# Kernel tuning notes

Hardware: AMD Instinct MI355X
Metric: run time of the kernel (lower is better)

The kernel has to match this reference:

```python
import jax, jax.numpy as jnp
import numpy as np

NUM_HEADS = 6

def setup_inputs() -> dict:
    key = jax.random.key(0)
    ks = jax.random.split(key, 6)
    B_, N, C = 4096, 64, 192
    nW = 4096
    return {
        "x": jax.random.normal(ks[0], (B_, N, C), dtype=jnp.float32),
        "mask": jax.random.normal(ks[1], (nW, N, N), dtype=jnp.float32),
        "qkv_w": jax.random.normal(ks[2], (3 * C, C), dtype=jnp.float32) * 0.02,
        "qkv_b": jax.random.normal(ks[3], (3 * C,), dtype=jnp.float32) * 0.02,
        "proj_w": jax.random.normal(ks[4], (C, C), dtype=jnp.float32) * 0.02,
        "proj_b": jax.random.normal(ks[5], (C,), dtype=jnp.float32) * 0.02,
    }

def reference(x, mask, qkv_w, qkv_b, proj_w, proj_b):
    B_, N, C = x.shape
    H = NUM_HEADS
    hd = C // H
    scale = hd ** -0.5
    qkv = (x @ qkv_w.T + qkv_b).reshape(B_, N, 3, H, hd)
    qkv = jnp.transpose(qkv, (2, 0, 3, 1, 4))  # [3, B_, H, N, hd]
    q, k, v = qkv[0], qkv[1], qkv[2]
    attn = jnp.einsum('bhnd,bhmd->bhnm', q * scale, k)  # [B_, H, N, N]
    nW = mask.shape[0]
    # additive relative/shift mask broadcast over image batch and heads
    attn = attn.reshape(B_ // nW, nW, H, N, N) + mask[None, :, None, :, :]
    attn = attn.reshape(B_, H, N, N)
    attn = jax.nn.softmax(attn, axis=-1)
    out = jnp.einsum('bhnm,bhmd->bhnd', attn, v)  # [B_, H, N, hd]
    out = jnp.transpose(out, (0, 2, 1, 3)).reshape(B_, N, C)
    return out @ proj_w.T + proj_b
```

## Files before the change

kernel.cpp:

```cpp
#include <hip/hip_runtime.h>
#include <hip/hip_bf16.h>
#include <stdint.h>


#define NTOK 64
#define CDIM 192
#define KVROW 72

typedef __attribute__((ext_vector_type(4))) float f32x4;
typedef __attribute__((ext_vector_type(8))) short bf16x8;

__device__ __forceinline__ short f2bf(float f) {
  __hip_bfloat16 h = __float2bfloat16(f);
  return *reinterpret_cast<short*>(&h);
}
__device__ __forceinline__ uint32_t pack2(float a, float b) {
  __hip_bfloat162 h2;
  h2.x = __float2bfloat16(a);
  h2.y = __float2bfloat16(b);
  return *reinterpret_cast<uint32_t*>(&h2);
}

__device__ __forceinline__ bf16x8 xpose(uint32_t A0, uint32_t A1,
                                        uint32_t B0, uint32_t B1,
                                        int s0, int s1, int hiSel) {
  uint32_t w[4];
  uint32_t a, b;
  a = (uint32_t)__shfl((int)A0, s0); b = (uint32_t)__shfl((int)B0, s0); w[0] = hiSel ? b : a;
  a = (uint32_t)__shfl((int)A1, s0); b = (uint32_t)__shfl((int)B1, s0); w[1] = hiSel ? b : a;
  a = (uint32_t)__shfl((int)A0, s1); b = (uint32_t)__shfl((int)B0, s1); w[2] = hiSel ? b : a;
  a = (uint32_t)__shfl((int)A1, s1); b = (uint32_t)__shfl((int)B1, s1); w[3] = hiSel ? b : a;
  return *reinterpret_cast<bf16x8*>(w);
}

#define GLOAD16(g, l) __builtin_amdgcn_global_load_lds( \
    (const __attribute__((address_space(1))) void*)(g), \
    (__attribute__((address_space(3))) void*)(l), 16, 0, 0)

__global__ void wconv_kernel(const float* __restrict__ qkv_w,
                             const float* __restrict__ proj_w,
                             short* __restrict__ ws) {
  const int r = blockIdx.x, c = threadIdx.x;
  int chunk, lr;
  float val;
  if (r < 192)      { chunk = r >> 6;                     lr = r & 63;          val = qkv_w[r * CDIM + c]; }
  else if (r < 384) { int q = r - 192; chunk = 3 + 2 * (q >> 6); lr = q & 63;   val = qkv_w[r * CDIM + c]; }
  else if (r < 576) { int q = r - 384; chunk = 4 + 2 * (q >> 6); lr = q & 63;   val = qkv_w[r * CDIM + c]; }
  else              { int q = r - 576; chunk = 9 + (q >> 6);     lr = q & 63;   val = proj_w[q * CDIM + c]; }
  const int s = c >> 3, lo = c & 7;
  const int sp = (s & 24) | ((s ^ lr) & 7);
  ws[chunk * 12288 + lr * CDIM + sp * 8 + lo] = f2bf(val);
}

__device__ __forceinline__ void stage_issue(short* __restrict__ wbuf,
                                            const short* __restrict__ src, int tid) {
  const int w = tid >> 6, lane = tid & 63;
  #pragma unroll
  for (int it = 0; it < 6; ++it) {
    const int cidx = it * 4 + w;
    GLOAD16(src + cidx * 512 + lane * 8, wbuf + cidx * 512);
  }
}

__global__ __launch_bounds__(256, 4)
void winattn_kernel(const float* __restrict__ x, const float* __restrict__ mask,
                    const short* __restrict__ ws,
                    const float* __restrict__ qkv_b, const float* __restrict__ proj_b,
                    float* __restrict__ out) {
  __shared__ __align__(16) short wbuf[64 * CDIM];
  __shared__ __align__(16) short khv[NTOK * KVROW];

  const int b    = blockIdx.x;
  const int tid  = threadIdx.x;
  const int lane = tid & 63;
  const int l16  = lane & 15;
  const int g4   = lane >> 4;
  const int m0   = (tid >> 6) * 16;
  const float scale = 0.17677669529663687f;
  const int s0 = (((2 * g4) & 3) << 4) + l16;
  const int s1 = (((2 * g4 + 1) & 3) << 4) + l16;
  const int hiSel = g4 >> 1;

  int soff[6];
  #pragma unroll
  for (int ks = 0; ks < 6; ++ks) {
    const int s = ks * 4 + g4;
    soff[ks] = ((s & 24) | ((s ^ l16) & 7)) << 3;
  }

  stage_issue(wbuf, ws, tid);

  const float* xr = x + (size_t)b * (NTOK * CDIM) + (m0 + l16) * CDIM;
  bf16x8 af[6];
  #pragma unroll
  for (int ks = 0; ks < 6; ++ks) {
    const float4 v0 = *reinterpret_cast<const float4*>(xr + ks * 32 + g4 * 8);
    const float4 v1 = *reinterpret_cast<const float4*>(xr + ks * 32 + g4 * 8 + 4);
    uint32_t t[4];
    t[0] = pack2(v0.x, v0.y); t[1] = pack2(v0.z, v0.w);
    t[2] = pack2(v1.x, v1.y); t[3] = pack2(v1.z, v1.w);
    af[ks] = *reinterpret_cast<bf16x8*>(t);
  }
  const float* mrowl = mask + (size_t)b * (NTOK * NTOK) + (m0 + l16) * NTOK;

  __syncthreads();

  bf16x8 aq[6];
  #pragma unroll
  for (int c = 0; c < 3; ++c) {
    uint32_t u[4][2];
    #pragma unroll
    for (int lct = 0; lct < 4; ++lct) {
      f32x4 acc = {0.f, 0.f, 0.f, 0.f};
      #pragma unroll
      for (int ks = 0; ks < 6; ++ks) {
        bf16x8 wf = *reinterpret_cast<const bf16x8*>(wbuf + (lct * 16 + l16) * CDIM + soff[ks]);
        acc = __builtin_amdgcn_mfma_f32_16x16x32_bf16(wf, af[ks], acc, 0, 0, 0);
      }
      const float4 bq = *reinterpret_cast<const float4*>(qkv_b + 64 * c + 16 * lct + 4 * g4);
      u[lct][0] = pack2((acc[0] + bq.x) * scale, (acc[1] + bq.y) * scale);
      u[lct][1] = pack2((acc[2] + bq.z) * scale, (acc[3] + bq.w) * scale);
    }
    __syncthreads();
    stage_issue(wbuf, ws + (c < 2 ? (c + 1) : 3) * 12288, tid);
    aq[2 * c]     = xpose(u[0][0], u[0][1], u[1][0], u[1][1], s0, s1, hiSel);
    aq[2 * c + 1] = xpose(u[2][0], u[2][1], u[3][0], u[3][1], s0, s1, hiSel);
    __syncthreads();
  }

  bf16x8 of[6];
  #pragma unroll
  for (int p = 0; p < 3; ++p) {
    #pragma unroll
    for (int lct = 0; lct < 4; ++lct) {
      f32x4 acc = {0.f, 0.f, 0.f, 0.f};
      #pragma unroll
      for (int ks = 0; ks < 6; ++ks) {
        bf16x8 wf = *reinterpret_cast<const bf16x8*>(wbuf + (lct * 16 + l16) * CDIM + soff[ks]);
        acc = __builtin_amdgcn_mfma_f32_16x16x32_bf16(wf, af[ks], acc, 0, 0, 0);
      }
      const float4 bk4 = *reinterpret_cast<const float4*>(qkv_b + 192 + 64 * p + 16 * lct + 4 * g4);
      uint2 kw;
      kw.x = pack2(acc[0] + bk4.x, acc[1] + bk4.y);
      kw.y = pack2(acc[2] + bk4.z, acc[3] + bk4.w);
      *reinterpret_cast<uint2*>(khv + (m0 + l16) * KVROW + 16 * lct + 4 * g4) = kw;
    }
    __syncthreads();
    stage_issue(wbuf, ws + (4 + 2 * p) * 12288, tid);

    float4 mreg[4];
    #pragma unroll
    for (int rt = 0; rt < 4; ++rt)
      mreg[rt] = *reinterpret_cast<const float4*>(mrowl + 16 * rt + 4 * g4);

    bf16x8 bp[2][2];
    #pragma unroll
    for (int e = 0; e < 2; ++e) {
      float pr[4][4];
      float rmax = -1e30f;
      #pragma unroll
      for (int rt = 0; rt < 4; ++rt) {
        bf16x8 bk = *reinterpret_cast<const bf16x8*>(khv + (rt * 16 + l16) * KVROW + 32 * e + g4 * 8);
        f32x4 z = {0.f, 0.f, 0.f, 0.f};
        f32x4 s = __builtin_amdgcn_mfma_f32_16x16x32_bf16(bk, aq[2 * p + e], z, 0, 0, 0);
        pr[rt][0] = s[0] + mreg[rt].x; pr[rt][1] = s[1] + mreg[rt].y;
        pr[rt][2] = s[2] + mreg[rt].z; pr[rt][3] = s[3] + mreg[rt].w;
        #pragma unroll
        for (int i = 0; i < 4; ++i) rmax = fmaxf(rmax, pr[rt][i]);
      }
      rmax = fmaxf(rmax, __shfl_xor(rmax, 16));
      rmax = fmaxf(rmax, __shfl_xor(rmax, 32));
      float rsum = 0.f;
      #pragma unroll
      for (int rt = 0; rt < 4; ++rt)
        #pragma unroll
        for (int i = 0; i < 4; ++i) { pr[rt][i] = __expf(pr[rt][i] - rmax); rsum += pr[rt][i]; }
      rsum += __shfl_xor(rsum, 16);
      rsum += __shfl_xor(rsum, 32);
      const float rinv = 1.f / rsum;
      uint32_t wpk[4][2];
      #pragma unroll
      for (int rt = 0; rt < 4; ++rt) {
        wpk[rt][0] = pack2(pr[rt][0] * rinv, pr[rt][1] * rinv);
        wpk[rt][1] = pack2(pr[rt][2] * rinv, pr[rt][3] * rinv);
      }
      bp[e][0] = xpose(wpk[0][0], wpk[0][1], wpk[1][0], wpk[1][1], s0, s1, hiSel);
      bp[e][1] = xpose(wpk[2][0], wpk[2][1], wpk[3][0], wpk[3][1], s0, s1, hiSel);
    }
    __syncthreads();

    #pragma unroll
    for (int lct = 0; lct < 4; ++lct) {
      f32x4 acc = {0.f, 0.f, 0.f, 0.f};
      #pragma unroll
      for (int ks = 0; ks < 6; ++ks) {
        bf16x8 wf = *reinterpret_cast<const bf16x8*>(wbuf + (lct * 16 + l16) * CDIM + soff[ks]);
        acc = __builtin_amdgcn_mfma_f32_16x16x32_bf16(af[ks], wf, acc, 0, 0, 0);
      }
      const float bv = qkv_b[384 + 64 * p + 16 * lct + l16];
      uint2 vw;
      vw.x = pack2(acc[0] + bv, acc[1] + bv);
      vw.y = pack2(acc[2] + bv, acc[3] + bv);
      *reinterpret_cast<uint2*>(khv + (16 * lct + l16) * KVROW + m0 + 4 * g4) = vw;
    }
    __syncthreads();
    stage_issue(wbuf, ws + (p < 2 ? (5 + 2 * p) : 9) * 12288, tid);

    #pragma unroll
    for (int e = 0; e < 2; ++e) {
      uint32_t uo[2][2];
      #pragma unroll
      for (int ct2 = 0; ct2 < 2; ++ct2) {
        const short* vb = khv + (32 * e + 16 * ct2 + l16) * KVROW;
        bf16x8 bv1 = *reinterpret_cast<const bf16x8*>(vb + g4 * 8);
        bf16x8 bv2 = *reinterpret_cast<const bf16x8*>(vb + 32 + g4 * 8);
        f32x4 acc = {0.f, 0.f, 0.f, 0.f};
        acc = __builtin_amdgcn_mfma_f32_16x16x32_bf16(bv1, bp[e][0], acc, 0, 0, 0);
        acc = __builtin_amdgcn_mfma_f32_16x16x32_bf16(bv2, bp[e][1], acc, 0, 0, 0);
        uo[ct2][0] = pack2(acc[0], acc[1]);
        uo[ct2][1] = pack2(acc[2], acc[3]);
      }
      of[2 * p + e] = xpose(uo[0][0], uo[0][1], uo[1][0], uo[1][1], s0, s1, hiSel);
    }
    __syncthreads();
  }

  float* og = out + (size_t)b * (NTOK * CDIM);
  #pragma unroll
  for (int c = 0; c < 3; ++c) {
    f32x4 acc[4];
    #pragma unroll
    for (int lct = 0; lct < 4; ++lct) {
      f32x4 a = {0.f, 0.f, 0.f, 0.f};
      #pragma unroll
      for (int ks = 0; ks < 6; ++ks) {
        bf16x8 wf = *reinterpret_cast<const bf16x8*>(wbuf + (lct * 16 + l16) * CDIM + soff[ks]);
        a = __builtin_amdgcn_mfma_f32_16x16x32_bf16(of[ks], wf, a, 0, 0, 0);
      }
      acc[lct] = a;
    }
    if (c < 2) {
      __syncthreads();
      stage_issue(wbuf, ws + (10 + c) * 12288, tid);
    }
    #pragma unroll
    for (int lct = 0; lct < 4; ++lct) {
      const int cc = 64 * c + 16 * lct + l16;
      const float pb = proj_b[cc];
      #pragma unroll
      for (int i = 0; i < 4; ++i)
        og[(m0 + 4 * g4 + i) * CDIM + cc] = acc[lct][i] + pb;
    }
    if (c < 2) __syncthreads();
  }
}

extern "C" void kernel_launch(void* const* d_in, const int* in_sizes, int n_in,
                              void* d_out, int out_size, void* d_ws, size_t ws_size,
                              hipStream_t stream) {
  const float* x      = (const float*)d_in[0];
  const float* mask   = (const float*)d_in[1];
  const float* qkv_w  = (const float*)d_in[2];
  const float* qkv_b  = (const float*)d_in[3];
  const float* proj_w = (const float*)d_in[4];
  const float* proj_b = (const float*)d_in[5];
  float* out = (float*)d_out;

  short* ws = (short*)d_ws;

  wconv_kernel<<<768, 192, 0, stream>>>(qkv_w, proj_w, ws);
  winattn_kernel<<<4096, 256, 0, stream>>>(x, mask, ws, qkv_b, proj_b, out);
}
```

Measured before the change: 243.4 us.

## Double-buffer 32-row weight chunks and pipeline per-head attention with PV overlap

Splits each 64-row staged weight chunk into two 32-row halves held in ping-pong LDS buffers, so the next chunk's global-to-LDS load overlaps compute on the current one. The attention loop now runs per head instead of per head pair, with a double-buffered V-transpose area, and defers each head's PV product into the next iteration to cut barriers. LDS use is roughly the same, but there are more loop iterations, more syncthreads calls and more small load issues, which could offset the overlap gain.

```diff
diff --git a/kernel.cpp b/kernel.cpp
--- a/kernel.cpp
+++ b/kernel.cpp
@@ -5,7 +5,8 @@
 
 #define NTOK 64
 #define CDIM 192
-#define KVROW 72
+#define KROW 40
+#define VROW 72
 
 typedef __attribute__((ext_vector_type(4))) float f32x4;
 typedef __attribute__((ext_vector_type(8))) short bf16x8;
@@ -43,22 +44,22 @@
   const int r = blockIdx.x, c = threadIdx.x;
   int chunk, lr;
   float val;
-  if (r < 192)      { chunk = r >> 6;                     lr = r & 63;          val = qkv_w[r * CDIM + c]; }
-  else if (r < 384) { int q = r - 192; chunk = 3 + 2 * (q >> 6); lr = q & 63;   val = qkv_w[r * CDIM + c]; }
-  else if (r < 576) { int q = r - 384; chunk = 4 + 2 * (q >> 6); lr = q & 63;   val = qkv_w[r * CDIM + c]; }
-  else              { int q = r - 576; chunk = 9 + (q >> 6);     lr = q & 63;   val = proj_w[q * CDIM + c]; }
+  if (r < 192)      { chunk = r >> 5;                        lr = r & 31;         val = qkv_w[r * CDIM + c]; }
+  else if (r < 384) { int q = r - 192; chunk = 6 + 2 * (q >> 5); lr = q & 31;     val = qkv_w[r * CDIM + c]; }
+  else if (r < 576) { int q = r - 384; chunk = 7 + 2 * (q >> 5); lr = q & 31;     val = qkv_w[r * CDIM + c]; }
+  else              { int q = r - 576; chunk = 18 + (q >> 5);    lr = q & 31;     val = proj_w[q * CDIM + c]; }
   const int s = c >> 3, lo = c & 7;
   const int sp = (s & 24) | ((s ^ lr) & 7);
-  ws[chunk * 12288 + lr * CDIM + sp * 8 + lo] = f2bf(val);
-}
-
-__device__ __forceinline__ void stage_issue(short* __restrict__ wbuf,
-                                            const short* __restrict__ src, int tid) {
+  ws[chunk * 6144 + lr * CDIM + sp * 8 + lo] = f2bf(val);
+}
+
+__device__ __forceinline__ void stage32(short* __restrict__ dst,
+                                        const short* __restrict__ src, int tid) {
   const int w = tid >> 6, lane = tid & 63;
   #pragma unroll
-  for (int it = 0; it < 6; ++it) {
+  for (int it = 0; it < 3; ++it) {
     const int cidx = it * 4 + w;
-    GLOAD16(src + cidx * 512 + lane * 8, wbuf + cidx * 512);
+    GLOAD16(src + cidx * 512 + lane * 8, dst + cidx * 512);
   }
 }
 
@@ -67,8 +68,10 @@
                     const short* __restrict__ ws,
                     const float* __restrict__ qkv_b, const float* __restrict__ proj_b,
                     float* __restrict__ out) {
-  __shared__ __align__(16) short wbuf[64 * CDIM];
-  __shared__ __align__(16) short khv[NTOK * KVROW];
+  __shared__ __align__(16) short wbA[32 * CDIM];
+  __shared__ __align__(16) short wbB[32 * CDIM];
+  __shared__ __align__(16) short kh[NTOK * KROW];
+  __shared__ __align__(16) short vth[2][32 * VROW];
 
   const int b    = blockIdx.x;
   const int tid  = threadIdx.x;
@@ -88,7 +91,8 @@
     soff[ks] = ((s & 24) | ((s ^ l16) & 7)) << 3;
   }
 
-  stage_issue(wbuf, ws, tid);
+  stage32(wbA, ws, tid);
+  stage32(wbB, ws + 6144, tid);
 
   const float* xr = x + (size_t)b * (NTOK * CDIM) + (m0 + l16) * CDIM;
   bf16x8 af[6];
@@ -107,64 +111,88 @@
 
   bf16x8 aq[6];
   #pragma unroll
-  for (int c = 0; c < 3; ++c) {
-    uint32_t u[4][2];
-    #pragma unroll
-    for (int lct = 0; lct < 4; ++lct) {
-      f32x4 acc = {0.f, 0.f, 0.f, 0.f};
-      #pragma unroll
-      for (int ks = 0; ks < 6; ++ks) {
-        bf16x8 wf = *reinterpret_cast<const bf16x8*>(wbuf + (lct * 16 + l16) * CDIM + soff[ks]);
+  for (int c = 0; c < 6; ++c) {
+    short* wb = (c & 1) ? wbB : wbA;
+    uint32_t u[2][2];
+    #pragma unroll
+    for (int lct = 0; lct < 2; ++lct) {
+      f32x4 acc = {0.f, 0.f, 0.f, 0.f};
+      #pragma unroll
+      for (int ks = 0; ks < 6; ++ks) {
+        bf16x8 wf = *reinterpret_cast<const bf16x8*>(wb + (lct * 16 + l16) * CDIM + soff[ks]);
         acc = __builtin_amdgcn_mfma_f32_16x16x32_bf16(wf, af[ks], acc, 0, 0, 0);
       }
-      const float4 bq = *reinterpret_cast<const float4*>(qkv_b + 64 * c + 16 * lct + 4 * g4);
+      const float4 bq = *reinterpret_cast<const float4*>(qkv_b + 32 * c + 16 * lct + 4 * g4);
       u[lct][0] = pack2((acc[0] + bq.x) * scale, (acc[1] + bq.y) * scale);
       u[lct][1] = pack2((acc[2] + bq.z) * scale, (acc[3] + bq.w) * scale);
     }
+    aq[c] = xpose(u[0][0], u[0][1], u[1][0], u[1][1], s0, s1, hiSel);
     __syncthreads();
-    stage_issue(wbuf, ws + (c < 2 ? (c + 1) : 3) * 12288, tid);
-    aq[2 * c]     = xpose(u[0][0], u[0][1], u[1][0], u[1][1], s0, s1, hiSel);
-    aq[2 * c + 1] = xpose(u[2][0], u[2][1], u[3][0], u[3][1], s0, s1, hiSel);
-    __syncthreads();
+    stage32(wb, ws + (c + 2) * 6144, tid);
   }
 
   bf16x8 of[6];
-  #pragma unroll
-  for (int p = 0; p < 3; ++p) {
-    #pragma unroll
-    for (int lct = 0; lct < 4; ++lct) {
-      f32x4 acc = {0.f, 0.f, 0.f, 0.f};
-      #pragma unroll
-      for (int ks = 0; ks < 6; ++ks) {
-        bf16x8 wf = *reinterpret_cast<const bf16x8*>(wbuf + (lct * 16 + l16) * CDIM + soff[ks]);
+  bf16x8 bpa, bpb;
+  #pragma unroll
+  for (int h = 0; h < 6; ++h) {
+    #pragma unroll
+    for (int lct = 0; lct < 2; ++lct) {
+      f32x4 acc = {0.f, 0.f, 0.f, 0.f};
+      #pragma unroll
+      for (int ks = 0; ks < 6; ++ks) {
+        bf16x8 wf = *reinterpret_cast<const bf16x8*>(wbA + (lct * 16 + l16) * CDIM + soff[ks]);
         acc = __builtin_amdgcn_mfma_f32_16x16x32_bf16(wf, af[ks], acc, 0, 0, 0);
       }
-      const float4 bk4 = *reinterpret_cast<const float4*>(qkv_b + 192 + 64 * p + 16 * lct + 4 * g4);
+      const float4 bk4 = *reinterpret_cast<const float4*>(qkv_b + 192 + 32 * h + 16 * lct + 4 * g4);
       uint2 kw;
       kw.x = pack2(acc[0] + bk4.x, acc[1] + bk4.y);
       kw.y = pack2(acc[2] + bk4.z, acc[3] + bk4.w);
-      *reinterpret_cast<uint2*>(khv + (m0 + l16) * KVROW + 16 * lct + 4 * g4) = kw;
+      *reinterpret_cast<uint2*>(kh + (m0 + l16) * KROW + 16 * lct + 4 * g4) = kw;
+    }
+    if (h > 0) {
+      const int vp = (h - 1) & 1;
+      uint32_t uo[2][2];
+      #pragma unroll
+      for (int ct2 = 0; ct2 < 2; ++ct2) {
+        const short* vb = vth[vp] + (16 * ct2 + l16) * VROW;
+        bf16x8 bv1 = *reinterpret_cast<const bf16x8*>(vb + g4 * 8);
+        bf16x8 bv2 = *reinterpret_cast<const bf16x8*>(vb + 32 + g4 * 8);
+        f32x4 acc = {0.f, 0.f, 0.f, 0.f};
+        acc = __builtin_amdgcn_mfma_f32_16x16x32_bf16(bv1, bpa, acc, 0, 0, 0);
+        acc = __builtin_amdgcn_mfma_f32_16x16x32_bf16(bv2, bpb, acc, 0, 0, 0);
+        uo[ct2][0] = pack2(acc[0], acc[1]);
+        uo[ct2][1] = pack2(acc[2], acc[3]);
+      }
+      of[h - 1] = xpose(uo[0][0], uo[0][1], uo[1][0], uo[1][1], s0, s1, hiSel);
     }
     __syncthreads();
-    stage_issue(wbuf, ws + (4 + 2 * p) * 12288, tid);
-
-    float4 mreg[4];
-    #pragma unroll
-    for (int rt = 0; rt < 4; ++rt)
-      mreg[rt] = *reinterpret_cast<const float4*>(mrowl + 16 * rt + 4 * g4);
-
-    bf16x8 bp[2][2];
-    #pragma unroll
-    for (int e = 0; e < 2; ++e) {
+    stage32(wbA, ws + (8 + 2 * h) * 6144, tid);
+
+    #pragma unroll
+    for (int lct = 0; lct < 2; ++lct) {
+      f32x4 acc = {0.f, 0.f, 0.f, 0.f};
+      #pragma unroll
+      for (int ks = 0; ks < 6; ++ks) {
+        bf16x8 wf = *reinterpret_cast<const bf16x8*>(wbB + (lct * 16 + l16) * CDIM + soff[ks]);
+        acc = __builtin_amdgcn_mfma_f32_16x16x32_bf16(af[ks], wf, acc, 0, 0, 0);
+      }
+      const float bv = qkv_b[384 + 32 * h + 16 * lct + l16];
+      uint2 vw;
+      vw.x = pack2(acc[0] + bv, acc[1] + bv);
+      vw.y = pack2(acc[2] + bv, acc[3] + bv);
+      *reinterpret_cast<uint2*>(vth[h & 1] + (16 * lct + l16) * VROW + m0 + 4 * g4) = vw;
+    }
+    {
       float pr[4][4];
       float rmax = -1e30f;
       #pragma unroll
       for (int rt = 0; rt < 4; ++rt) {
-        bf16x8 bk = *reinterpret_cast<const bf16x8*>(khv + (rt * 16 + l16) * KVROW + 32 * e + g4 * 8);
+        bf16x8 bk = *reinterpret_cast<const bf16x8*>(kh + (rt * 16 + l16) * KROW + g4 * 8);
         f32x4 z = {0.f, 0.f, 0.f, 0.f};
-        f32x4 s = __builtin_amdgcn_mfma_f32_16x16x32_bf16(bk, aq[2 * p + e], z, 0, 0, 0);
-        pr[rt][0] = s[0] + mreg[rt].x; pr[rt][1] = s[1] + mreg[rt].y;
-        pr[rt][2] = s[2] + mreg[rt].z; pr[rt][3] = s[3] + mreg[rt].w;
+        f32x4 s = __builtin_amdgcn_mfma_f32_16x16x32_bf16(bk, aq[h], z, 0, 0, 0);
+        const float4 mv = *reinterpret_cast<const float4*>(mrowl + 16 * rt + 4 * g4);
+        pr[rt][0] = s[0] + mv.x; pr[rt][1] = s[1] + mv.y;
+        pr[rt][2] = s[2] + mv.z; pr[rt][3] = s[3] + mv.w;
         #pragma unroll
         for (int i = 0; i < 4; ++i) rmax = fmaxf(rmax, pr[rt][i]);
       }
@@ -184,74 +212,51 @@
         wpk[rt][0] = pack2(pr[rt][0] * rinv, pr[rt][1] * rinv);
         wpk[rt][1] = pack2(pr[rt][2] * rinv, pr[rt][3] * rinv);
       }
-      bp[e][0] = xpose(wpk[0][0], wpk[0][1], wpk[1][0], wpk[1][1], s0, s1, hiSel);
-      bp[e][1] = xpose(wpk[2][0], wpk[2][1], wpk[3][0], wpk[3][1], s0, s1, hiSel);
+      bpa = xpose(wpk[0][0], wpk[0][1], wpk[1][0], wpk[1][1], s0, s1, hiSel);
+      bpb = xpose(wpk[2][0], wpk[2][1], wpk[3][0], wpk[3][1], s0, s1, hiSel);
     }
     __syncthreads();
-
-    #pragma unroll
-    for (int lct = 0; lct < 4; ++lct) {
-      f32x4 acc = {0.f, 0.f, 0.f, 0.f};
-      #pragma unroll
-      for (int ks = 0; ks < 6; ++ks) {
-        bf16x8 wf = *reinterpret_cast<const bf16x8*>(wbuf + (lct * 16 + l16) * CDIM + soff[ks]);
-        acc = __builtin_amdgcn_mfma_f32_16x16x32_bf16(af[ks], wf, acc, 0, 0, 0);
-      }
-      const float bv = qkv_b[384 + 64 * p + 16 * lct + l16];
-      uint2 vw;
-      vw.x = pack2(acc[0] + bv, acc[1] + bv);
-      vw.y = pack2(acc[2] + bv, acc[3] + bv);
-      *reinterpret_cast<uint2*>(khv + (16 * lct + l16) * KVROW + m0 + 4 * g4) = vw;
-    }
-    __syncthreads();
-    stage_issue(wbuf, ws + (p < 2 ? (5 + 2 * p) : 9) * 12288, tid);
-
-    #pragma unroll
-    for (int e = 0; e < 2; ++e) {
+    stage32(wbB, ws + (9 + 2 * h) * 6144, tid);
+  }
+
+  float* og = out + (size_t)b * (NTOK * CDIM);
+  #pragma unroll
+  for (int j = 0; j < 6; ++j) {
+    const int c = 18 + j;
+    short* wb = (c & 1) ? wbB : wbA;
+    if (j == 0) {
       uint32_t uo[2][2];
       #pragma unroll
       for (int ct2 = 0; ct2 < 2; ++ct2) {
-        const short* vb = khv + (32 * e + 16 * ct2 + l16) * KVROW;
+        const short* vb = vth[1] + (16 * ct2 + l16) * VROW;
         bf16x8 bv1 = *reinterpret_cast<const bf16x8*>(vb + g4 * 8);
         bf16x8 bv2 = *reinterpret_cast<const bf16x8*>(vb + 32 + g4 * 8);
         f32x4 acc = {0.f, 0.f, 0.f, 0.f};
-        acc = __builtin_amdgcn_mfma_f32_16x16x32_bf16(bv1, bp[e][0], acc, 0, 0, 0);
-        acc = __builtin_amdgcn_mfma_f32_16x16x32_bf16(bv2, bp[e][1], acc, 0, 0, 0);
+        acc = __builtin_amdgcn_mfma_f32_16x16x32_bf16(bv1, bpa, acc, 0, 0, 0);
+        acc = __builtin_amdgcn_mfma_f32_16x16x32_bf16(bv2, bpb, acc, 0, 0, 0);
         uo[ct2][0] = pack2(acc[0], acc[1]);
         uo[ct2][1] = pack2(acc[2], acc[3]);
       }
-      of[2 * p + e] = xpose(uo[0][0], uo[0][1], uo[1][0], uo[1][1], s0, s1, hiSel);
-    }
-    __syncthreads();
-  }
-
-  float* og = out + (size_t)b * (NTOK * CDIM);
-  #pragma unroll
-  for (int c = 0; c < 3; ++c) {
-    f32x4 acc[4];
-    #pragma unroll
-    for (int lct = 0; lct < 4; ++lct) {
-      f32x4 a = {0.f, 0.f, 0.f, 0.f};
-      #pragma unroll
-      for (int ks = 0; ks < 6; ++ks) {
-        bf16x8 wf = *reinterpret_cast<const bf16x8*>(wbuf + (lct * 16 + l16) * CDIM + soff[ks]);
-        a = __builtin_amdgcn_mfma_f32_16x16x32_bf16(of[ks], wf, a, 0, 0, 0);
-      }
-      acc[lct] = a;
-    }
-    if (c < 2) {
+      of[5] = xpose(uo[0][0], uo[0][1], uo[1][0], uo[1][1], s0, s1, hiSel);
+    }
+    #pragma unroll
+    for (int lct = 0; lct < 2; ++lct) {
+      f32x4 acc = {0.f, 0.f, 0.f, 0.f};
+      #pragma unroll
+      for (int ks = 0; ks < 6; ++ks) {
+        bf16x8 wf = *reinterpret_cast<const bf16x8*>(wb + (lct * 16 + l16) * CDIM + soff[ks]);
+        acc = __builtin_amdgcn_mfma_f32_16x16x32_bf16(of[ks], wf, acc, 0, 0, 0);
+      }
+      const int cc = 32 * j + 16 * lct + l16;
+      const float pb = proj_b[cc];
+      #pragma unroll
+      for (int i = 0; i < 4; ++i)
+        og[(m0 + 4 * g4 + i) * CDIM + cc] = acc[i] + pb;
+    }
+    if (j < 5) {
       __syncthreads();
-      stage_issue(wbuf, ws + (10 + c) * 12288, tid);
-    }
-    #pragma unroll
-    for (int lct = 0; lct < 4; ++lct) {
-      const int cc = 64 * c + 16 * lct + l16;
-      const float pb = proj_b[cc];
-      #pragma unroll
-      for (int i = 0; i < 4; ++i)
-        og[(m0 + 4 * g4 + i) * CDIM + cc] = acc[lct][i] + pb;
-    }
-    if (c < 2) __syncthreads();
+      if (j < 4) stage32(wb, ws + (c + 2) * 6144, tid);
+    }
   }
 }
 
```

Measured after the change: 231.1 us. -5.1%, faster.
